# Kernel optimization log

Measured on AMD Instinct MI355X. Metric: run time of the kernel, lower is better.

Reference implementation:

```python
import jax, jax.numpy as jnp
import numpy as np


def _leaky(x):
    return jnp.where(x >= 0, x, 0.01 * x)  # nn.LeakyReLU default slope


def _conv1x1(x, w):
    # x: [B, C, H, W], w: [O, C] (1x1 conv == per-pixel channel GEMM)
    return jnp.einsum('bchw,oc->bohw', x, w)


def setup_inputs() -> dict:
    key = jax.random.key(0)
    ks = jax.random.split(key, 12)

    def kaiming(k, o, c):  # kaiming_normal_ fan_out, relu gain, 1x1 kernel
        return jax.random.normal(k, (o, c), jnp.float32) * np.float32(np.sqrt(2.0 / o))

    lr_feature = jax.random.normal(ks[0], (1, 32, 256, 512), jnp.float32)
    hr_feature = jax.random.normal(ks[1], (1, 32, 512, 1024), jnp.float32)
    return {
        'lr_feature': lr_feature,
        'hr_feature': hr_feature,
        's1_w0': kaiming(ks[2], 128, 128),
        's1_w1': kaiming(ks[3], 64, 128),
        's1_w2': kaiming(ks[4], 32, 64),
        's1_w3': kaiming(ks[5], 16, 32),
        's1_w4': kaiming(ks[6], 8, 16),
        's1_w5': kaiming(ks[7], 1, 8),
        's2_w0': kaiming(ks[8], 3, 3),
        's2_w1': kaiming(ks[9], 2, 3),
        's2_w2': kaiming(ks[10], 1, 2),
        'fuse_w': jnp.ones((1, 2), jnp.float32),  # fuse weight initialized to 1
    }


def reference(lr_feature, hr_feature, s1_w0, s1_w1, s1_w2, s1_w3, s1_w4, s1_w5,
              s2_w0, s2_w1, s2_w2, fuse_w):
    scale = hr_feature.shape[-1] // lr_feature.shape[-1]  # static python int (=2, even)
    Hh, Wh = hr_feature.shape[-2], hr_feature.shape[-1]

    # nearest-neighbor upsample of lr_feature by `scale` (expand/view trick in torch)
    lr_up = jnp.repeat(jnp.repeat(lr_feature, scale, axis=2), scale, axis=3)

    # representation: [B, 128, Hh, Wh]
    rep = jnp.concatenate(
        [lr_up, hr_feature, lr_up * hr_feature, (lr_up - hr_feature) ** 2], axis=1)

    # similarity_measure1: 1x1-conv MLP chain 128->128->64->32->16->8->1
    o = _leaky(_conv1x1(rep, s1_w0))
    o = _leaky(_conv1x1(o, s1_w1))
    o = _leaky(_conv1x1(o, s1_w2))
    o = _leaky(_conv1x1(o, s1_w3))
    o = _conv1x1(o, s1_w4)
    weights1 = _conv1x1(o, s1_w5)  # [B, 1, Hh, Wh]

    # distance matrix (even-scale branch): 3 channels [dx, dy, norm]
    v = jnp.arange(-(scale // 2), scale // 2 + 1, dtype=jnp.float32)
    m = v.shape[0] // 2
    v = jnp.concatenate([v[:m], v[m + 1:]])  # drop center -> length `scale`
    d0 = jnp.broadcast_to(v[None, :], (scale, scale))
    dm = jnp.stack([d0, d0.T, jnp.sqrt(d0 ** 2 + d0.T ** 2)], axis=0)  # [3,s,s]
    dm = jnp.tile(dm, (1, Hh // scale, Wh // scale))[None]  # [1, 3, Hh, Wh]

    # similarity_measure2: 3->3->2->1
    w2 = _leaky(_conv1x1(dm, s2_w0))
    w2 = _leaky(_conv1x1(w2, s2_w1))
    weights2 = _conv1x1(w2, s2_w2)  # [1, 1, Hh, Wh]

    # fuse (weight forced non-negative via abs, as in forward's .data mutation)
    mapping = _conv1x1(jnp.concatenate([weights1, weights2], axis=1), jnp.abs(fuse_w))
    return mapping
```

## Files before the change

kernel.cpp:

```cpp
#include <hip/hip_runtime.h>

typedef short v8s __attribute__((ext_vector_type(8)));
typedef float v4f __attribute__((ext_vector_type(4)));

#define Wh   1024
#define Hh   512
#define HWh  (Wh * Hh)
#define Wlr  512
#define HWlr (Wlr * 256)
#define PAD  136
#define ITERS 8
#define NBLK  256

#define WFRAG_SHORTS (53 * 512)
#define ACT_SHORTS   (16 * PAD)
#define LDS_BYTES    ((WFRAG_SHORTS + 16 * ACT_SHORTS) * 2)

__device__ __forceinline__ unsigned short f2bf(float f) {
    union { float f; unsigned u; } v; v.f = f;
    unsigned r = v.u + 0x7FFFu + ((v.u >> 16) & 1u);
    return (unsigned short)(r >> 16);
}
__device__ __forceinline__ unsigned pk2(float a, float b) {
    union { float f; unsigned u; } ua, ub;
    ua.f = a; ub.f = b;
    return __builtin_amdgcn_perm(ub.u + 0x8000u, ua.u + 0x8000u, 0x07060302u);
}
__device__ __forceinline__ float leaky(float x) { return fmaxf(x, 0.01f * x); }

__device__ __forceinline__ void ld16(const float* __restrict__ hr, const float* __restrict__ lr,
                                     int gbase, int p, int q,
                                     float (&h)[4][2], float (&l)[4][2]) {
    const int y  = gbase >> 10;
    const int xg = (gbase & 1023) + p;
    const float* hb = hr + (size_t)y * Wh + xg;
    const float* lb = lr + (size_t)(y >> 1) * Wlr + (xg >> 1);
#pragma unroll
    for (int pass = 0; pass < 4; ++pass) {
        const int ch = pass * 8 + q * 2;
        h[pass][0] = hb[(size_t)ch * HWh];
        h[pass][1] = hb[(size_t)(ch + 1) * HWh];
        l[pass][0] = lb[(size_t)ch * HWlr];
        l[pass][1] = lb[(size_t)(ch + 1) * HWlr];
    }
}

__global__ __launch_bounds__(1024, 4)
void cmfsm_kernel(const float* __restrict__ lr, const float* __restrict__ hr,
                  const float* __restrict__ w0g, const float* __restrict__ w1g,
                  const float* __restrict__ w2g, const float* __restrict__ w3g,
                  const float* __restrict__ w4g, const float* __restrict__ w5g,
                  const float* __restrict__ t0g, const float* __restrict__ t1g,
                  const float* __restrict__ t2g, const float* __restrict__ fwg,
                  float* __restrict__ out)
{
    extern __shared__ unsigned short smem[];
    unsigned short* wfrag = smem;
    unsigned short* actS  = smem + WFRAG_SHORTS;

    const int tid  = threadIdx.x;
    const int lane = tid & 63;
    const int wv   = tid >> 6;
    const int p    = lane & 15;
    const int q    = lane >> 4;

    for (int e = tid; e < 32 * 64; e += 1024) {
        int f = e >> 6, l = e & 63;
        int mt = f >> 2, ks = f & 3, pp = l & 15, qq = l >> 4;
        const float* src = w0g + (mt * 16 + pp) * 128 + ks * 32 + qq * 8;
        unsigned short* dst = wfrag + f * 512 + l * 8;
#pragma unroll
        for (int j = 0; j < 8; ++j) dst[j] = f2bf(src[j]);
    }
    if (tid < 16 * 64) {
        int f = tid >> 6, l = tid & 63;
        int mt = f >> 2, ks = f & 3, pp = l & 15, qq = l >> 4;
        const float* src = w1g + (mt * 16 + pp) * 128 + ks * 32 + qq * 8;
        unsigned short* dst = wfrag + (32 + f) * 512 + l * 8;
#pragma unroll
        for (int j = 0; j < 8; ++j) dst[j] = f2bf(src[j]);
    }
    if (tid < 4 * 64) {
        int f = tid >> 6, l = tid & 63;
        int mt = f >> 1, ks = f & 1, pp = l & 15, qq = l >> 4;
        const float* src = w2g + (mt * 16 + pp) * 64 + ks * 32 + qq * 8;
        unsigned short* dst = wfrag + (48 + f) * 512 + l * 8;
#pragma unroll
        for (int j = 0; j < 8; ++j) dst[j] = f2bf(src[j]);
    }
    if (tid < 64) {
        int l = tid;
        int pp = l & 15, qq = l >> 4;
        const float* src = w3g + pp * 32 + qq * 8;
        unsigned short* dst = wfrag + 52 * 512 + l * 8;
#pragma unroll
        for (int j = 0; j < 8; ++j) dst[j] = f2bf(src[j]);
    }

    float w45[4];
#pragma unroll
    for (int r = 0; r < 4; ++r) {
        float s = 0.f;
#pragma unroll
        for (int j = 0; j < 8; ++j) s += w5g[j] * w4g[j * 16 + q * 4 + r];
        w45[r] = s;
    }

    float w2tab[4];
#pragma unroll
    for (int yp = 0; yp < 2; ++yp)
#pragma unroll
        for (int xp = 0; xp < 2; ++xp) {
            float i0 = xp ? 1.f : -1.f;
            float i1 = yp ? 1.f : -1.f;
            float i2 = 1.41421356237309505f;
            float h0[3], h1[2];
            for (int o = 0; o < 3; ++o)
                h0[o] = leaky(t0g[o*3+0]*i0 + t0g[o*3+1]*i1 + t0g[o*3+2]*i2);
            for (int o = 0; o < 2; ++o)
                h1[o] = leaky(t1g[o*3+0]*h0[0] + t1g[o*3+1]*h0[1] + t1g[o*3+2]*h0[2]);
            w2tab[yp*2+xp] = t2g[0]*h1[0] + t2g[1]*h1[1];
        }
    const float fa = fabsf(fwg[0]);
    const float fb = fabsf(fwg[1]);

    __syncthreads();

    unsigned short* A = actS + wv * ACT_SHORTS;

    float ph[4][2], pl[4][2];
    ld16(hr, lr, (blockIdx.x * ITERS) * 256 + wv * 16, p, q, ph, pl);

#pragma unroll 1
    for (int it = 0; it < ITERS; ++it) {
        const int gbase = (blockIdx.x * ITERS + it) * 256 + wv * 16;
        const int y     = gbase >> 10;
        const int xg    = (gbase & 1023) + p;

#pragma unroll
        for (int pass = 0; pass < 4; ++pass) {
            int ch = pass * 8 + q * 2;
            float h0 = ph[pass][0], h1 = ph[pass][1];
            float l0 = pl[pass][0], l1 = pl[pass][1];
            unsigned* Ap = (unsigned*)(A + p * PAD);
            Ap[ch >> 1]        = pk2(l0, l1);
            Ap[(32 + ch) >> 1] = pk2(h0, h1);
            Ap[(64 + ch) >> 1] = pk2(l0 * h0, l1 * h1);
            float d0 = l0 - h0, d1 = l1 - h1;
            Ap[(96 + ch) >> 1] = pk2(d0 * d0, d1 * d1);
        }

        const int nit = (it + 1 < ITERS) ? it + 1 : it;
        ld16(hr, lr, (blockIdx.x * ITERS + nit) * 256 + wv * 16, p, q, ph, pl);

        v4f acc0[8];
#pragma unroll
        for (int mt = 0; mt < 8; ++mt) acc0[mt] = (v4f){0.f, 0.f, 0.f, 0.f};
#pragma unroll
        for (int ks = 0; ks < 4; ++ks) {
            v8s b = *(const v8s*)(A + p * PAD + ks * 32 + q * 8);
#pragma unroll
            for (int mt = 0; mt < 8; ++mt) {
                v8s a = *(const v8s*)(wfrag + (mt * 4 + ks) * 512 + lane * 8);
                acc0[mt] = __builtin_amdgcn_mfma_f32_16x16x32_bf16(a, b, acc0[mt], 0, 0, 0);
            }
        }
#pragma unroll
        for (int mt = 0; mt < 8; ++mt) {
            uint2 v;
            v.x = pk2(leaky(acc0[mt][0]), leaky(acc0[mt][1]));
            v.y = pk2(leaky(acc0[mt][2]), leaky(acc0[mt][3]));
            *(uint2*)(A + p * PAD + mt * 16 + q * 4) = v;
        }

        v4f acc1[4];
#pragma unroll
        for (int mt = 0; mt < 4; ++mt) acc1[mt] = (v4f){0.f, 0.f, 0.f, 0.f};
#pragma unroll
        for (int ks = 0; ks < 4; ++ks) {
            v8s b = *(const v8s*)(A + p * PAD + ks * 32 + q * 8);
#pragma unroll
            for (int mt = 0; mt < 4; ++mt) {
                v8s a = *(const v8s*)(wfrag + (32 + mt * 4 + ks) * 512 + lane * 8);
                acc1[mt] = __builtin_amdgcn_mfma_f32_16x16x32_bf16(a, b, acc1[mt], 0, 0, 0);
            }
        }
#pragma unroll
        for (int mt = 0; mt < 4; ++mt) {
            uint2 v;
            v.x = pk2(leaky(acc1[mt][0]), leaky(acc1[mt][1]));
            v.y = pk2(leaky(acc1[mt][2]), leaky(acc1[mt][3]));
            *(uint2*)(A + p * PAD + mt * 16 + q * 4) = v;
        }

        v4f acc2[2];
#pragma unroll
        for (int mt = 0; mt < 2; ++mt) acc2[mt] = (v4f){0.f, 0.f, 0.f, 0.f};
#pragma unroll
        for (int ks = 0; ks < 2; ++ks) {
            v8s b = *(const v8s*)(A + p * PAD + ks * 32 + q * 8);
#pragma unroll
            for (int mt = 0; mt < 2; ++mt) {
                v8s a = *(const v8s*)(wfrag + (48 + mt * 2 + ks) * 512 + lane * 8);
                acc2[mt] = __builtin_amdgcn_mfma_f32_16x16x32_bf16(a, b, acc2[mt], 0, 0, 0);
            }
        }
#pragma unroll
        for (int mt = 0; mt < 2; ++mt) {
            uint2 v;
            v.x = pk2(leaky(acc2[mt][0]), leaky(acc2[mt][1]));
            v.y = pk2(leaky(acc2[mt][2]), leaky(acc2[mt][3]));
            *(uint2*)(A + p * PAD + mt * 16 + q * 4) = v;
        }

        {
            v8s b = *(const v8s*)(A + p * PAD + q * 8);
            v8s a = *(const v8s*)(wfrag + 52 * 512 + lane * 8);
            v4f acc3 = __builtin_amdgcn_mfma_f32_16x16x32_bf16(a, b, (v4f){0.f, 0.f, 0.f, 0.f}, 0, 0, 0);

            float part = 0.f;
#pragma unroll
            for (int r = 0; r < 4; ++r) part += w45[r] * leaky(acc3[r]);
            part += __shfl_xor(part, 16, 64);
            part += __shfl_xor(part, 32, 64);

            if (q == 0) {
                float res = fa * part + fb * w2tab[(y & 1) * 2 + (xg & 1)];
                out[y * Wh + xg] = res;
            }
        }
    }
}

extern "C" void kernel_launch(void* const* d_in, const int* in_sizes, int n_in,
                              void* d_out, int out_size, void* d_ws, size_t ws_size,
                              hipStream_t stream) {
    const float* lr  = (const float*)d_in[0];
    const float* hr  = (const float*)d_in[1];
    const float* w0g = (const float*)d_in[2];
    const float* w1g = (const float*)d_in[3];
    const float* w2g = (const float*)d_in[4];
    const float* w3g = (const float*)d_in[5];
    const float* w4g = (const float*)d_in[6];
    const float* w5g = (const float*)d_in[7];
    const float* t0g = (const float*)d_in[8];
    const float* t1g = (const float*)d_in[9];
    const float* t2g = (const float*)d_in[10];
    const float* fwg = (const float*)d_in[11];
    float* out = (float*)d_out;

    hipLaunchKernelGGL(cmfsm_kernel, dim3(NBLK), dim3(1024), LDS_BYTES, stream,
                       lr, hr, w0g, w1g, w2g, w3g, w4g, w5g, t0g, t1g, t2g, fwg, out);
}
```

Baseline: 150.7 us.

## Build first-layer MFMA operands in registers instead of staging through LDS

Each lane now loads 8 consecutive channels of hr/lr for its pixel and packs the four representation blocks (lr, hr, product, squared difference) straight into MFMA B-operand registers. This removes the LDS write and read-back of the 128-channel input before the first GEMM. The loop is restructured into row/segment iterations with incrementing base pointers and row parity known at compile time. Layer 0 is also split into two halves to cap accumulator register pressure. In exchange, each lane holds more global loads in flight, and each half reloads the B operand choice from registers.

```diff
diff --git a/kernel.cpp b/kernel.cpp
--- a/kernel.cpp
+++ b/kernel.cpp
@@ -2,6 +2,7 @@
 
 typedef short v8s __attribute__((ext_vector_type(8)));
 typedef float v4f __attribute__((ext_vector_type(4)));
+typedef unsigned v4u __attribute__((ext_vector_type(4)));
 
 #define Wh   1024
 #define Hh   512
@@ -27,23 +28,6 @@
     return __builtin_amdgcn_perm(ub.u + 0x8000u, ua.u + 0x8000u, 0x07060302u);
 }
 __device__ __forceinline__ float leaky(float x) { return fmaxf(x, 0.01f * x); }
-
-__device__ __forceinline__ void ld16(const float* __restrict__ hr, const float* __restrict__ lr,
-                                     int gbase, int p, int q,
-                                     float (&h)[4][2], float (&l)[4][2]) {
-    const int y  = gbase >> 10;
-    const int xg = (gbase & 1023) + p;
-    const float* hb = hr + (size_t)y * Wh + xg;
-    const float* lb = lr + (size_t)(y >> 1) * Wlr + (xg >> 1);
-#pragma unroll
-    for (int pass = 0; pass < 4; ++pass) {
-        const int ch = pass * 8 + q * 2;
-        h[pass][0] = hb[(size_t)ch * HWh];
-        h[pass][1] = hb[(size_t)(ch + 1) * HWh];
-        l[pass][0] = lb[(size_t)ch * HWlr];
-        l[pass][1] = lb[(size_t)(ch + 1) * HWlr];
-    }
-}
 
 __global__ __launch_bounds__(1024, 4)
 void cmfsm_kernel(const float* __restrict__ lr, const float* __restrict__ hr,
@@ -106,127 +90,168 @@
         w45[r] = s;
     }
 
-    float w2tab[4];
-#pragma unroll
-    for (int yp = 0; yp < 2; ++yp)
-#pragma unroll
-        for (int xp = 0; xp < 2; ++xp) {
-            float i0 = xp ? 1.f : -1.f;
-            float i1 = yp ? 1.f : -1.f;
-            float i2 = 1.41421356237309505f;
-            float h0[3], h1[2];
-            for (int o = 0; o < 3; ++o)
-                h0[o] = leaky(t0g[o*3+0]*i0 + t0g[o*3+1]*i1 + t0g[o*3+2]*i2);
-            for (int o = 0; o < 2; ++o)
-                h1[o] = leaky(t1g[o*3+0]*h0[0] + t1g[o*3+1]*h0[1] + t1g[o*3+2]*h0[2]);
-            w2tab[yp*2+xp] = t2g[0]*h1[0] + t2g[1]*h1[1];
-        }
+    float w2t0, w2t1, w2t2, w2t3;
+    {
+        float tab[4];
+#pragma unroll
+        for (int yp = 0; yp < 2; ++yp)
+#pragma unroll
+            for (int xp = 0; xp < 2; ++xp) {
+                float i0 = xp ? 1.f : -1.f;
+                float i1 = yp ? 1.f : -1.f;
+                float i2 = 1.41421356237309505f;
+                float h0[3], h1[2];
+                for (int o = 0; o < 3; ++o)
+                    h0[o] = leaky(t0g[o*3+0]*i0 + t0g[o*3+1]*i1 + t0g[o*3+2]*i2);
+                for (int o = 0; o < 2; ++o)
+                    h1[o] = leaky(t1g[o*3+0]*h0[0] + t1g[o*3+1]*h0[1] + t1g[o*3+2]*h0[2]);
+                tab[yp*2+xp] = t2g[0]*h1[0] + t2g[1]*h1[1];
+            }
+        w2t0 = tab[0]; w2t1 = tab[1]; w2t2 = tab[2]; w2t3 = tab[3];
+    }
     const float fa = fabsf(fwg[0]);
     const float fb = fabsf(fwg[1]);
 
     __syncthreads();
 
-    unsigned short* A = actS + wv * ACT_SHORTS;
-
-    float ph[4][2], pl[4][2];
-    ld16(hr, lr, (blockIdx.x * ITERS) * 256 + wv * 16, p, q, ph, pl);
+    unsigned short* Arow = actS + wv * ACT_SHORTS + p * PAD;
+    const unsigned short* ARq8 = Arow + q * 8;
+    unsigned short* AWq4       = Arow + q * 4;
+    const unsigned short* WL   = wfrag + lane * 8;
+
+    const float* hrp[8];
+    const float* lrp[8];
+    {
+        const int hbase = blockIdx.x * 2048 + wv * 16 + p;
+        const int lbase = blockIdx.x * 512  + wv * 8  + (p >> 1);
+#pragma unroll
+        for (int j = 0; j < 8; ++j) {
+            hrp[j] = hr + (size_t)(q * 8 + j) * HWh  + hbase;
+            lrp[j] = lr + (size_t)(q * 8 + j) * HWlr + lbase;
+        }
+    }
+
+    float h[8], l[8];
+#pragma unroll
+    for (int j = 0; j < 8; ++j) { h[j] = hrp[j][0]; l[j] = lrp[j][0]; }
 
 #pragma unroll 1
-    for (int it = 0; it < ITERS; ++it) {
-        const int gbase = (blockIdx.x * ITERS + it) * 256 + wv * 16;
-        const int y     = gbase >> 10;
-        const int xg    = (gbase & 1023) + p;
-
-#pragma unroll
-        for (int pass = 0; pass < 4; ++pass) {
-            int ch = pass * 8 + q * 2;
-            float h0 = ph[pass][0], h1 = ph[pass][1];
-            float l0 = pl[pass][0], l1 = pl[pass][1];
-            unsigned* Ap = (unsigned*)(A + p * PAD);
-            Ap[ch >> 1]        = pk2(l0, l1);
-            Ap[(32 + ch) >> 1] = pk2(h0, h1);
-            Ap[(64 + ch) >> 1] = pk2(l0 * h0, l1 * h1);
-            float d0 = l0 - h0, d1 = l1 - h1;
-            Ap[(96 + ch) >> 1] = pk2(d0 * d0, d1 * d1);
-        }
-
-        const int nit = (it + 1 < ITERS) ? it + 1 : it;
-        ld16(hr, lr, (blockIdx.x * ITERS + nit) * 256 + wv * 16, p, q, ph, pl);
-
-        v4f acc0[8];
-#pragma unroll
-        for (int mt = 0; mt < 8; ++mt) acc0[mt] = (v4f){0.f, 0.f, 0.f, 0.f};
-#pragma unroll
-        for (int ks = 0; ks < 4; ++ks) {
-            v8s b = *(const v8s*)(A + p * PAD + ks * 32 + q * 8);
-#pragma unroll
-            for (int mt = 0; mt < 8; ++mt) {
-                v8s a = *(const v8s*)(wfrag + (mt * 4 + ks) * 512 + lane * 8);
-                acc0[mt] = __builtin_amdgcn_mfma_f32_16x16x32_bf16(a, b, acc0[mt], 0, 0, 0);
-            }
-        }
-#pragma unroll
-        for (int mt = 0; mt < 8; ++mt) {
-            uint2 v;
-            v.x = pk2(leaky(acc0[mt][0]), leaky(acc0[mt][1]));
-            v.y = pk2(leaky(acc0[mt][2]), leaky(acc0[mt][3]));
-            *(uint2*)(A + p * PAD + mt * 16 + q * 4) = v;
-        }
-
-        v4f acc1[4];
-#pragma unroll
-        for (int mt = 0; mt < 4; ++mt) acc1[mt] = (v4f){0.f, 0.f, 0.f, 0.f};
-#pragma unroll
-        for (int ks = 0; ks < 4; ++ks) {
-            v8s b = *(const v8s*)(A + p * PAD + ks * 32 + q * 8);
-#pragma unroll
-            for (int mt = 0; mt < 4; ++mt) {
-                v8s a = *(const v8s*)(wfrag + (32 + mt * 4 + ks) * 512 + lane * 8);
-                acc1[mt] = __builtin_amdgcn_mfma_f32_16x16x32_bf16(a, b, acc1[mt], 0, 0, 0);
-            }
-        }
-#pragma unroll
-        for (int mt = 0; mt < 4; ++mt) {
-            uint2 v;
-            v.x = pk2(leaky(acc1[mt][0]), leaky(acc1[mt][1]));
-            v.y = pk2(leaky(acc1[mt][2]), leaky(acc1[mt][3]));
-            *(uint2*)(A + p * PAD + mt * 16 + q * 4) = v;
-        }
-
-        v4f acc2[2];
-#pragma unroll
-        for (int mt = 0; mt < 2; ++mt) acc2[mt] = (v4f){0.f, 0.f, 0.f, 0.f};
-#pragma unroll
-        for (int ks = 0; ks < 2; ++ks) {
-            v8s b = *(const v8s*)(A + p * PAD + ks * 32 + q * 8);
-#pragma unroll
-            for (int mt = 0; mt < 2; ++mt) {
-                v8s a = *(const v8s*)(wfrag + (48 + mt * 2 + ks) * 512 + lane * 8);
-                acc2[mt] = __builtin_amdgcn_mfma_f32_16x16x32_bf16(a, b, acc2[mt], 0, 0, 0);
-            }
-        }
-#pragma unroll
-        for (int mt = 0; mt < 2; ++mt) {
-            uint2 v;
-            v.x = pk2(leaky(acc2[mt][0]), leaky(acc2[mt][1]));
-            v.y = pk2(leaky(acc2[mt][2]), leaky(acc2[mt][3]));
-            *(uint2*)(A + p * PAD + mt * 16 + q * 4) = v;
-        }
-
-        {
-            v8s b = *(const v8s*)(A + p * PAD + q * 8);
-            v8s a = *(const v8s*)(wfrag + 52 * 512 + lane * 8);
-            v4f acc3 = __builtin_amdgcn_mfma_f32_16x16x32_bf16(a, b, (v4f){0.f, 0.f, 0.f, 0.f}, 0, 0, 0);
-
-            float part = 0.f;
-#pragma unroll
-            for (int r = 0; r < 4; ++r) part += w45[r] * leaky(acc3[r]);
-            part += __shfl_xor(part, 16, 64);
-            part += __shfl_xor(part, 32, 64);
-
-            if (q == 0) {
-                float res = fa * part + fb * w2tab[(y & 1) * 2 + (xg & 1)];
-                out[y * Wh + xg] = res;
+    for (int t = 0; t < 2; ++t) {
+#pragma unroll
+        for (int s = 0; s < 4; ++s) {
+            v4u bf0, bf1, bf2, bf3;
+#pragma unroll
+            for (int u = 0; u < 4; ++u) {
+                float l0 = l[2*u], l1 = l[2*u+1];
+                float h0 = h[2*u], h1 = h[2*u+1];
+                bf0[u] = pk2(l0, l1);
+                bf1[u] = pk2(h0, h1);
+                bf2[u] = pk2(l0 * h0, l1 * h1);
+                float d0 = l0 - h0, d1 = l1 - h1;
+                bf3[u] = pk2(d0 * d0, d1 * d1);
+            }
+            v8s b0 = __builtin_bit_cast(v8s, bf0);
+            v8s b1 = __builtin_bit_cast(v8s, bf1);
+            v8s b2 = __builtin_bit_cast(v8s, bf2);
+            v8s b3 = __builtin_bit_cast(v8s, bf3);
+
+#pragma unroll
+            for (int j = 0; j < 8; ++j) hrp[j] += 256;
+            if (t == 0 || s < 3) {
+                const int nlr = ((s + 1) & 3) * 128;
+#pragma unroll
+                for (int j = 0; j < 8; ++j) {
+                    h[j] = hrp[j][0];
+                    l[j] = lrp[j][nlr];
+                }
+            }
+
+#pragma unroll
+            for (int half = 0; half < 2; ++half) {
+                v4f acc[4];
+#pragma unroll
+                for (int m2 = 0; m2 < 4; ++m2) acc[m2] = (v4f){0.f, 0.f, 0.f, 0.f};
+#pragma unroll
+                for (int ks = 0; ks < 4; ++ks) {
+                    v8s b = (ks == 0) ? b0 : (ks == 1) ? b1 : (ks == 2) ? b2 : b3;
+#pragma unroll
+                    for (int m2 = 0; m2 < 4; ++m2) {
+                        const int mt = half * 4 + m2;
+                        v8s a = *(const v8s*)(WL + (mt * 4 + ks) * 512);
+                        acc[m2] = __builtin_amdgcn_mfma_f32_16x16x32_bf16(a, b, acc[m2], 0, 0, 0);
+                    }
+                }
+#pragma unroll
+                for (int m2 = 0; m2 < 4; ++m2) {
+                    const int mt = half * 4 + m2;
+                    uint2 v;
+                    v.x = pk2(leaky(acc[m2][0]), leaky(acc[m2][1]));
+                    v.y = pk2(leaky(acc[m2][2]), leaky(acc[m2][3]));
+                    *(uint2*)(AWq4 + mt * 16) = v;
+                }
+            }
+
+            {
+                v4f acc1[4];
+#pragma unroll
+                for (int mt = 0; mt < 4; ++mt) acc1[mt] = (v4f){0.f, 0.f, 0.f, 0.f};
+#pragma unroll
+                for (int ks = 0; ks < 4; ++ks) {
+                    v8s b = *(const v8s*)(ARq8 + ks * 32);
+#pragma unroll
+                    for (int mt = 0; mt < 4; ++mt) {
+                        v8s a = *(const v8s*)(WL + (32 + mt * 4 + ks) * 512);
+                        acc1[mt] = __builtin_amdgcn_mfma_f32_16x16x32_bf16(a, b, acc1[mt], 0, 0, 0);
+                    }
+                }
+#pragma unroll
+                for (int mt = 0; mt < 4; ++mt) {
+                    uint2 v;
+                    v.x = pk2(leaky(acc1[mt][0]), leaky(acc1[mt][1]));
+                    v.y = pk2(leaky(acc1[mt][2]), leaky(acc1[mt][3]));
+                    *(uint2*)(AWq4 + mt * 16) = v;
+                }
+            }
+
+            {
+                v4f acc2[2];
+#pragma unroll
+                for (int mt = 0; mt < 2; ++mt) acc2[mt] = (v4f){0.f, 0.f, 0.f, 0.f};
+#pragma unroll
+                for (int ks = 0; ks < 2; ++ks) {
+                    v8s b = *(const v8s*)(ARq8 + ks * 32);
+#pragma unroll
+                    for (int mt = 0; mt < 2; ++mt) {
+                        v8s a = *(const v8s*)(WL + (48 + mt * 2 + ks) * 512);
+                        acc2[mt] = __builtin_amdgcn_mfma_f32_16x16x32_bf16(a, b, acc2[mt], 0, 0, 0);
+                    }
+                }
+#pragma unroll
+                for (int mt = 0; mt < 2; ++mt) {
+                    uint2 v;
+                    v.x = pk2(leaky(acc2[mt][0]), leaky(acc2[mt][1]));
+                    v.y = pk2(leaky(acc2[mt][2]), leaky(acc2[mt][3]));
+                    *(uint2*)(AWq4 + mt * 16) = v;
+                }
+            }
+
+            {
+                v8s b = *(const v8s*)(ARq8);
+                v8s a = *(const v8s*)(WL + 52 * 512);
+                v4f acc3 = __builtin_amdgcn_mfma_f32_16x16x32_bf16(a, b, (v4f){0.f, 0.f, 0.f, 0.f}, 0, 0, 0);
+
+                float part = 0.f;
+#pragma unroll
+                for (int r = 0; r < 4; ++r) part += w45[r] * leaky(acc3[r]);
+                part += __shfl_xor(part, 16, 64);
+                part += __shfl_xor(part, 32, 64);
+
+                if (q == 0) {
+                    const float w2v = t ? ((p & 1) ? w2t3 : w2t2)
+                                        : ((p & 1) ? w2t1 : w2t0);
+                    const int gidx = blockIdx.x * 2048 + (t * 4 + s) * 256 + wv * 16 + p;
+                    out[gidx] = fa * part + fb * w2v;
+                }
             }
         }
     }
```

Result: no change. 149.6 us (-0.7%).
